# Kernel tuning notes

Hardware: AMD Instinct MI355X
Metric: run time of the kernel (lower is better)

## Reference

```python
import jax, jax.numpy as jnp
import numpy as np

NB_CLASSES = 2048
SZ_EMBED = 128
N = 16384
TAU = 32.0
ALPHA = 0.9


def setup_inputs() -> dict:
    key = jax.random.key(0)
    k1, k2, k3 = jax.random.split(key, 3)
    X = jax.random.normal(k1, (N, SZ_EMBED), dtype=jnp.float32)
    # labels: arange % C guarantees every class occurs in the batch, so the
    # torch code's dynamic class_within_batch selection == all classes.
    T = jnp.arange(N, dtype=jnp.int64) % NB_CLASSES
    # kaiming_normal_(mode='fan_out') on [C,F]: std = sqrt(2/C)
    std = float(np.sqrt(2.0 / NB_CLASSES))
    means = jax.random.normal(k2, (NB_CLASSES, SZ_EMBED), dtype=jnp.float32) * std
    log_vars = jax.random.normal(k3, (NB_CLASSES, SZ_EMBED), dtype=jnp.float32) * std
    return {"X": X, "T": T, "means": means, "log_vars": log_vars}


def _l2norm(x, eps=1e-12):
    return x / jnp.maximum(jnp.linalg.norm(x, axis=-1, keepdims=True), eps)


def reference(X, T, means, log_vars):
    # relu6 on log-variances (torch F.relu6)
    lv = jnp.clip(log_vars, 0.0, 6.0)                      # [C,F]
    Xn = _l2norm(X)                                        # [N,F]
    mu = _l2norm(means)                                    # [C,F]
    # Mahalanobis D[n,c] = sum_f (x-mu)^2 / exp(lv)
    # Expanded to GEMMs to avoid materializing [N,C,F]:
    inv_cov = jnp.exp(-lv)                                 # [C,F]
    D = (jnp.einsum('nf,cf->nc', Xn * Xn, inv_cov)
         - 2.0 * jnp.einsum('nf,cf->nc', Xn, mu * inv_cov)
         + jnp.sum(mu * mu * inv_cov, axis=-1)[None, :])   # [N,C]
    # softmax over classes; loss_n = -log p[n, T[n]] (softmax is strictly >0,
    # so the torch `non_zero` filter keeps every row)
    logp = jax.nn.log_softmax(-TAU * D, axis=1)            # [N,C]
    loss = -logp[jnp.arange(X.shape[0]), T]                # [N]
    loss_mean = jnp.mean(loss)
    # H over all classes (all classes present in batch)
    P = jax.nn.one_hot(T, NB_CLASSES, dtype=D.dtype)       # [N,C]
    H = P + jnp.exp(-ALPHA * D) * (1.0 - P)                # [N,C]
    return (loss_mean, H)
```

## Files before the change

kernel.cpp:

```cpp
#include <hip/hip_runtime.h>

#define C_CLASSES 2048
#define F_EMBED   128
#define N_ROWS    16384

constexpr float TAU    = 32.0f;
constexpr float ALPHA  = 0.9f;
constexpr float ZSHIFT = 64.0f;

typedef __bf16 bf16x8 __attribute__((ext_vector_type(8)));
typedef float  f32x4  __attribute__((ext_vector_type(4)));

__device__ __forceinline__ float wsum64(float v) {
#pragma unroll
  for (int m = 1; m < 64; m <<= 1) v += __shfl_xor(v, m, 64);
  return v;
}

__global__ __launch_bounds__(256) void prep_classes_k(
    const float* __restrict__ means, const float* __restrict__ log_vars,
    __bf16* __restrict__ icb, __bf16* __restrict__ w2b,
    float* __restrict__ s3, float* __restrict__ out0) {
  const int c    = blockIdx.x * 4 + (threadIdx.x >> 6);
  const int lane = threadIdx.x & 63;
  const size_t base = (size_t)c * F_EMBED;
  const float m0 = means[base + lane], m1 = means[base + lane + 64];
  const float ss = wsum64(m0 * m0 + m1 * m1);
  const float inv = 1.0f / fmaxf(sqrtf(ss), 1e-12f);
  const float mu0 = m0 * inv, mu1 = m1 * inv;
  const float lv0 = fminf(fmaxf(log_vars[base + lane], 0.0f), 6.0f);
  const float lv1 = fminf(fmaxf(log_vars[base + lane + 64], 0.0f), 6.0f);
  const float ic0 = __expf(-lv0), ic1 = __expf(-lv1);
  const float s3p = wsum64(mu0 * mu0 * ic0 + mu1 * mu1 * ic1);
  icb[base + lane]      = (__bf16)ic0;
  icb[base + lane + 64] = (__bf16)ic1;
  w2b[base + lane]      = (__bf16)(-2.0f * mu0 * ic0);
  w2b[base + lane + 64] = (__bf16)(-2.0f * mu1 * ic1);
  if (lane == 0) s3[c] = s3p;
  if (c == 0 && lane == 0) out0[0] = 0.0f;
}

__global__ __launch_bounds__(256) void prep_rows_k(
    const float* __restrict__ X, __bf16* __restrict__ xnb, __bf16* __restrict__ xn2b) {
  const int n    = blockIdx.x * 4 + (threadIdx.x >> 6);
  const int lane = threadIdx.x & 63;
  const size_t base = (size_t)n * F_EMBED;
  const float x0 = X[base + lane], x1 = X[base + lane + 64];
  const float ss = wsum64(x0 * x0 + x1 * x1);
  const float inv = 1.0f / fmaxf(sqrtf(ss), 1e-12f);
  const float a0 = x0 * inv, a1 = x1 * inv;
  xnb[base + lane]       = (__bf16)a0;
  xnb[base + lane + 64]  = (__bf16)a1;
  xn2b[base + lane]      = (__bf16)(a0 * a0);
  xn2b[base + lane + 64] = (__bf16)(a1 * a1);
}

__global__ __launch_bounds__(512, 2) void mahal_main_k(
    const __bf16* __restrict__ xnb, const __bf16* __restrict__ xn2b,
    const __bf16* __restrict__ icb, const __bf16* __restrict__ w2b,
    const float* __restrict__ s3, const int* __restrict__ T,
    float* __restrict__ out) {
  __shared__ int   Tl[64];
  __shared__ float LsLDS[8][64];
  __shared__ float DtLDS[8][64];
  const int tid  = threadIdx.x;
  const int w    = tid >> 6;
  const int lane = tid & 63;
  const int lo   = lane & 15;
  const int hi   = lane >> 4;
  const int rowbase = blockIdx.x * 64;
  if (tid < 64) Tl[tid] = T[rowbase + tid];
  __syncthreads();

  bf16x8 axn[4][4], ax2[4][4];
#pragma unroll
  for (int rg = 0; rg < 4; ++rg) {
#pragma unroll
    for (int kg = 0; kg < 4; ++kg) {
      const size_t off = (size_t)(rowbase + rg * 16 + lo) * F_EMBED + kg * 32 + hi * 8;
      axn[rg][kg] = *(const bf16x8*)(xnb + off);
      ax2[rg][kg] = *(const bf16x8*)(xn2b + off);
    }
  }
  int tT[4][4];
#pragma unroll
  for (int rg = 0; rg < 4; ++rg)
#pragma unroll
    for (int r = 0; r < 4; ++r) tT[rg][r] = Tl[rg * 16 + hi * 4 + r];

  float lsum[4][4], dTv[4][4];
#pragma unroll
  for (int rg = 0; rg < 4; ++rg)
#pragma unroll
    for (int r = 0; r < 4; ++r) { lsum[rg][r] = 0.0f; dTv[rg][r] = 0.0f; }

  const int cbase = w * 256;
  for (int ct = 0; ct < 16; ++ct) {
    const int cb  = cbase + ct * 16;
    const int col = cb + lo;
    f32x4 acc[4];
#pragma unroll
    for (int rg = 0; rg < 4; ++rg) acc[rg] = (f32x4){0.0f, 0.0f, 0.0f, 0.0f};
    const size_t cboff = (size_t)col * F_EMBED + hi * 8;
#pragma unroll
    for (int kg = 0; kg < 4; ++kg) {
      const bf16x8 bic = *(const bf16x8*)(icb + cboff + kg * 32);
      const bf16x8 bw2 = *(const bf16x8*)(w2b + cboff + kg * 32);
#pragma unroll
      for (int rg = 0; rg < 4; ++rg) {
        acc[rg] = __builtin_amdgcn_mfma_f32_16x16x32_bf16(ax2[rg][kg], bic, acc[rg], 0, 0, 0);
        acc[rg] = __builtin_amdgcn_mfma_f32_16x16x32_bf16(axn[rg][kg], bw2, acc[rg], 0, 0, 0);
      }
    }
    const float s3c = s3[col];
#pragma unroll
    for (int rg = 0; rg < 4; ++rg) {
#pragma unroll
      for (int r = 0; r < 4; ++r) {
        const float D   = acc[rg][r] + s3c;
        const int   row = rowbase + rg * 16 + hi * 4 + r;
        const bool  isT = (col == tT[rg][r]);
        const float h   = isT ? 1.0f : __expf(-ALPHA * D);
        out[1 + (size_t)row * C_CLASSES + col] = h;
        lsum[rg][r] += __expf(ZSHIFT - TAU * D);
        if (isT) dTv[rg][r] += D;
      }
    }
  }

#pragma unroll
  for (int rg = 0; rg < 4; ++rg) {
#pragma unroll
    for (int r = 0; r < 4; ++r) {
      float L = lsum[rg][r], Dv = dTv[rg][r];
#pragma unroll
      for (int m = 1; m < 16; m <<= 1) {
        L  += __shfl_xor(L, m, 64);
        Dv += __shfl_xor(Dv, m, 64);
      }
      if (lo == 0) {
        LsLDS[w][rg * 16 + hi * 4 + r] = L;
        DtLDS[w][rg * 16 + hi * 4 + r] = Dv;
      }
    }
  }
  __syncthreads();
  if (tid < 64) {
    float L = 0.0f, Dv = 0.0f;
#pragma unroll
    for (int ww = 0; ww < 8; ++ww) { L += LsLDS[ww][tid]; Dv += DtLDS[ww][tid]; }
    float loss = TAU * Dv + logf(L) - ZSHIFT;
    loss = wsum64(loss);
    if (tid == 0) atomicAdd(out, loss * (1.0f / N_ROWS));
  }
}

extern "C" void kernel_launch(void* const* d_in, const int* in_sizes, int n_in,
                              void* d_out, int out_size, void* d_ws, size_t ws_size,
                              hipStream_t stream) {
  const float* X        = (const float*)d_in[0];
  const int*   T        = (const int*)d_in[1];
  const float* means    = (const float*)d_in[2];
  const float* log_vars = (const float*)d_in[3];
  float* out = (float*)d_out;

  char* ws = (char*)d_ws;
  __bf16* icb  = (__bf16*)ws;
  __bf16* w2b  = (__bf16*)(ws + (512u << 10));
  float*  s3   = (float*)(ws + (1u << 20));
  __bf16* xnb  = (__bf16*)(ws + (1u << 20) + (16u << 10));
  __bf16* xn2b = (__bf16*)(ws + (1u << 20) + (16u << 10) + (4u << 20));

  prep_classes_k<<<C_CLASSES / 4, 256, 0, stream>>>(means, log_vars, icb, w2b, s3, out);
  prep_rows_k<<<N_ROWS / 4, 256, 0, stream>>>(X, xnb, xn2b);
  mahal_main_k<<<N_ROWS / 64, 512, 0, stream>>>(xnb, xn2b, icb, w2b, s3, T, out);
}
```

Measured before the change: 250.5 us.

## Transpose MFMA tiles so each lane writes contiguous H columns per row

Swaps the MFMA operand order so each lane owns one row and four consecutive class columns. This makes the H stores contiguous per row instead of strided across rows. Blocks shrink to 32 rows with 8 waves split into 2 row groups by 4 column quarters, and occupancy is raised to 4 blocks per CU. The next class tile is register-prefetched while the current MFMAs run, and s3 is loaded as a vector. The natural exps become exp2f with log2e folded into the constants. In exchange, class operands are re-read twice as often per output and register pressure under the tighter launch bound may spill.

```diff
diff --git a/kernel.cpp b/kernel.cpp
--- a/kernel.cpp
+++ b/kernel.cpp
@@ -5,8 +5,11 @@
 #define N_ROWS    16384
 
 constexpr float TAU    = 32.0f;
-constexpr float ALPHA  = 0.9f;
-constexpr float ZSHIFT = 64.0f;
+constexpr float LOG2E  = 1.4426950408889634f;
+constexpr float LN2    = 0.6931471805599453f;
+constexpr float TAU2   = TAU * LOG2E;
+constexpr float ZS2    = 64.0f * LOG2E;
+constexpr float AL2    = -0.9f * LOG2E;
 
 typedef __bf16 bf16x8 __attribute__((ext_vector_type(8)));
 typedef float  f32x4  __attribute__((ext_vector_type(4)));
@@ -55,103 +58,105 @@
   xn2b[base + lane + 64] = (__bf16)(a1 * a1);
 }
 
-__global__ __launch_bounds__(512, 2) void mahal_main_k(
+__global__ __launch_bounds__(512, 4) void mahal_main_k(
     const __bf16* __restrict__ xnb, const __bf16* __restrict__ xn2b,
     const __bf16* __restrict__ icb, const __bf16* __restrict__ w2b,
     const float* __restrict__ s3, const int* __restrict__ T,
     float* __restrict__ out) {
-  __shared__ int   Tl[64];
-  __shared__ float LsLDS[8][64];
-  __shared__ float DtLDS[8][64];
+  __shared__ int   Tl[32];
+  __shared__ float Ls[8][16];
+  __shared__ float Dt[8][16];
   const int tid  = threadIdx.x;
   const int w    = tid >> 6;
   const int lane = tid & 63;
   const int lo   = lane & 15;
   const int hi   = lane >> 4;
-  const int rowbase = blockIdx.x * 64;
-  if (tid < 64) Tl[tid] = T[rowbase + tid];
+  const int rowg = w & 1;
+  const int q    = w >> 1;
+  const int rowbase = blockIdx.x * 32;
+  if (tid < 32) Tl[tid] = T[rowbase + tid];
   __syncthreads();
 
-  bf16x8 axn[4][4], ax2[4][4];
-#pragma unroll
-  for (int rg = 0; rg < 4; ++rg) {
+  const int myrow = rowg * 16 + lo;
+  const int tTl   = Tl[myrow];
+
+  bf16x8 axn[4], ax2[4];
+  {
+    const size_t rb = (size_t)(rowbase + myrow) * F_EMBED + hi * 8;
 #pragma unroll
     for (int kg = 0; kg < 4; ++kg) {
-      const size_t off = (size_t)(rowbase + rg * 16 + lo) * F_EMBED + kg * 32 + hi * 8;
-      axn[rg][kg] = *(const bf16x8*)(xnb + off);
-      ax2[rg][kg] = *(const bf16x8*)(xn2b + off);
-    }
-  }
-  int tT[4][4];
-#pragma unroll
-  for (int rg = 0; rg < 4; ++rg)
-#pragma unroll
-    for (int r = 0; r < 4; ++r) tT[rg][r] = Tl[rg * 16 + hi * 4 + r];
-
-  float lsum[4][4], dTv[4][4];
-#pragma unroll
-  for (int rg = 0; rg < 4; ++rg)
-#pragma unroll
-    for (int r = 0; r < 4; ++r) { lsum[rg][r] = 0.0f; dTv[rg][r] = 0.0f; }
-
-  const int cbase = w * 256;
-  for (int ct = 0; ct < 16; ++ct) {
-    const int cb  = cbase + ct * 16;
-    const int col = cb + lo;
-    f32x4 acc[4];
-#pragma unroll
-    for (int rg = 0; rg < 4; ++rg) acc[rg] = (f32x4){0.0f, 0.0f, 0.0f, 0.0f};
-    const size_t cboff = (size_t)col * F_EMBED + hi * 8;
-#pragma unroll
-    for (int kg = 0; kg < 4; ++kg) {
-      const bf16x8 bic = *(const bf16x8*)(icb + cboff + kg * 32);
-      const bf16x8 bw2 = *(const bf16x8*)(w2b + cboff + kg * 32);
-#pragma unroll
-      for (int rg = 0; rg < 4; ++rg) {
-        acc[rg] = __builtin_amdgcn_mfma_f32_16x16x32_bf16(ax2[rg][kg], bic, acc[rg], 0, 0, 0);
-        acc[rg] = __builtin_amdgcn_mfma_f32_16x16x32_bf16(axn[rg][kg], bw2, acc[rg], 0, 0, 0);
-      }
-    }
-    const float s3c = s3[col];
-#pragma unroll
-    for (int rg = 0; rg < 4; ++rg) {
-#pragma unroll
-      for (int r = 0; r < 4; ++r) {
-        const float D   = acc[rg][r] + s3c;
-        const int   row = rowbase + rg * 16 + hi * 4 + r;
-        const bool  isT = (col == tT[rg][r]);
-        const float h   = isT ? 1.0f : __expf(-ALPHA * D);
-        out[1 + (size_t)row * C_CLASSES + col] = h;
-        lsum[rg][r] += __expf(ZSHIFT - TAU * D);
-        if (isT) dTv[rg][r] += D;
-      }
+      axn[kg] = *(const bf16x8*)(xnb  + rb + kg * 32);
+      ax2[kg] = *(const bf16x8*)(xn2b + rb + kg * 32);
     }
   }
 
+  float lsum = 0.0f, dTv = 0.0f;
+  float* __restrict__ outH = out + 1 + (size_t)(rowbase + myrow) * C_CLASSES;
+
+  bf16x8 cic[4], cw2[4];
+  {
+    const size_t cb = (size_t)(q * 64 + lo) * F_EMBED + hi * 8;
 #pragma unroll
-  for (int rg = 0; rg < 4; ++rg) {
+    for (int kg = 0; kg < 4; ++kg) {
+      cic[kg] = *(const bf16x8*)(icb + cb + kg * 32);
+      cw2[kg] = *(const bf16x8*)(w2b + cb + kg * 32);
+    }
+  }
+
+  for (int t = 0; t < 32; ++t) {
+    const int ctbase = (q + 4 * (t >> 2)) * 64 + (t & 3) * 16;
+
+    f32x4 acc = {0.f, 0.f, 0.f, 0.f};
+#pragma unroll
+    for (int kg = 0; kg < 4; ++kg) {
+      acc = __builtin_amdgcn_mfma_f32_16x16x32_bf16(cic[kg], ax2[kg], acc, 0, 0, 0);
+      acc = __builtin_amdgcn_mfma_f32_16x16x32_bf16(cw2[kg], axn[kg], acc, 0, 0, 0);
+    }
+
+    if (t < 31) {
+      const int t2 = t + 1;
+      const int nb = (q + 4 * (t2 >> 2)) * 64 + (t2 & 3) * 16;
+      const size_t cb = (size_t)(nb + lo) * F_EMBED + hi * 8;
+#pragma unroll
+      for (int kg = 0; kg < 4; ++kg) {
+        cic[kg] = *(const bf16x8*)(icb + cb + kg * 32);
+        cw2[kg] = *(const bf16x8*)(w2b + cb + kg * 32);
+      }
+    }
+
+    const f32x4 s3v = *(const f32x4*)(s3 + ctbase + hi * 4);
 #pragma unroll
     for (int r = 0; r < 4; ++r) {
-      float L = lsum[rg][r], Dv = dTv[rg][r];
-#pragma unroll
-      for (int m = 1; m < 16; m <<= 1) {
-        L  += __shfl_xor(L, m, 64);
-        Dv += __shfl_xor(Dv, m, 64);
-      }
-      if (lo == 0) {
-        LsLDS[w][rg * 16 + hi * 4 + r] = L;
-        DtLDS[w][rg * 16 + hi * 4 + r] = Dv;
-      }
+      const int   c   = ctbase + hi * 4 + r;
+      const float D   = acc[r] + s3v[r];
+      const bool  isT = (c == tTl);
+      outH[c] = isT ? 1.0f : exp2f(AL2 * D);
+      lsum += exp2f(ZS2 - TAU2 * D);
+      if (isT) dTv = D;
     }
   }
+
+  lsum += __shfl_xor(lsum, 16, 64);
+  lsum += __shfl_xor(lsum, 32, 64);
+  dTv  += __shfl_xor(dTv, 16, 64);
+  dTv  += __shfl_xor(dTv, 32, 64);
+  if (hi == 0) { Ls[w][lo] = lsum; Dt[w][lo] = dTv; }
   __syncthreads();
-  if (tid < 64) {
-    float L = 0.0f, Dv = 0.0f;
+
+  if (w == 0) {
+    float loss = 0.0f;
+    if (lane < 32) {
+      const int rr = lane & 15, rgg = lane >> 4;
+      float L = 0.f, Dv = 0.f;
 #pragma unroll
-    for (int ww = 0; ww < 8; ++ww) { L += LsLDS[ww][tid]; Dv += DtLDS[ww][tid]; }
-    float loss = TAU * Dv + logf(L) - ZSHIFT;
+      for (int qq = 0; qq < 4; ++qq) {
+        L  += Ls[2 * qq + rgg][rr];
+        Dv += Dt[2 * qq + rgg][rr];
+      }
+      loss = TAU * Dv + __log2f(L) * LN2 - 64.0f;
+    }
     loss = wsum64(loss);
-    if (tid == 0) atomicAdd(out, loss * (1.0f / N_ROWS));
+    if (lane == 0) atomicAdd(out, loss * (1.0f / N_ROWS));
   }
 }
 
@@ -173,5 +178,5 @@
 
   prep_classes_k<<<C_CLASSES / 4, 256, 0, stream>>>(means, log_vars, icb, w2b, s3, out);
   prep_rows_k<<<N_ROWS / 4, 256, 0, stream>>>(X, xnb, xn2b);
-  mahal_main_k<<<N_ROWS / 64, 512, 0, stream>>>(xnb, xn2b, icb, w2b, s3, T, out);
+  mahal_main_k<<<N_ROWS / 32, 512, 0, stream>>>(xnb, xn2b, icb, w2b, s3, T, out);
 }
```

After: 271.2 us. 8.2% more time.
